# Kernel tuning notes

Measured on AMD Instinct MI355X. Metric: run time of the kernel, lower is better.

## Reference

```python
import jax, jax.numpy as jnp
import numpy as np

DIM = 1280
HEADS = 8
DH = DIM // HEADS  # 160
CROSS = 768
FRAMES = 16
B = 2
TOK = 256        # spatial tokens per frame
ESEQ = 77
INNER = 4 * DIM  # 5120, geglu inner


def _ln(x, w, b):
    m = x.mean(-1, keepdims=True)
    v = x.var(-1, keepdims=True)
    return (x - m) / jnp.sqrt(v + 1e-5) * w + b


def _split_heads(x):
    Bt, S, C = x.shape
    return x.reshape(Bt, S, HEADS, C // HEADS).transpose(0, 2, 1, 3)


def _attn_core(q, k, v):
    # q,k,v: [B, S, C] -> multi-head attention -> [B, Sq, C]
    qh, kh, vh = _split_heads(q), _split_heads(k), _split_heads(v)
    scores = jnp.einsum('bhqd,bhkd->bhqk', qh, kh) * (DH ** -0.5)
    attn = jax.nn.softmax(scores, axis=-1)
    o = jnp.einsum('bhqk,bhkd->bhqd', attn, vh)
    Bt, H, S, Dh = o.shape
    return o.transpose(0, 2, 1, 3).reshape(Bt, S, H * Dh)


def setup_inputs() -> dict:
    key = jax.random.key(0)
    ks = jax.random.split(key, 32)
    s = 0.02

    def w(i, shape):
        return jax.random.normal(ks[i], shape, dtype=jnp.float32) * s

    inp = {
        'hidden_states': jax.random.normal(ks[0], (B * FRAMES, TOK, DIM), dtype=jnp.float32),
        'encoder_hidden_states': jax.random.normal(ks[1], (B * FRAMES, ESEQ, CROSS), dtype=jnp.float32),
        # norm1 / attn1 (sparse causal self-attn)
        'n1w': jnp.ones((DIM,), jnp.float32), 'n1b': jnp.zeros((DIM,), jnp.float32),
        'a1wq': w(2, (DIM, DIM)), 'a1wk': w(3, (DIM, DIM)), 'a1wv': w(4, (DIM, DIM)),
        'a1wo': w(5, (DIM, DIM)), 'a1bo': jnp.zeros((DIM,), jnp.float32),
        # norm2 / attn2 (cross)
        'n2w': jnp.ones((DIM,), jnp.float32), 'n2b': jnp.zeros((DIM,), jnp.float32),
        'a2wq': w(6, (DIM, DIM)), 'a2wk': w(7, (CROSS, DIM)), 'a2wv': w(8, (CROSS, DIM)),
        'a2wo': w(9, (DIM, DIM)), 'a2bo': jnp.zeros((DIM,), jnp.float32),
        # norm3 / geglu FFN
        'n3w': jnp.ones((DIM,), jnp.float32), 'n3b': jnp.zeros((DIM,), jnp.float32),
        'ffw1': w(10, (DIM, 2 * INNER)), 'ffb1': jnp.zeros((2 * INNER,), jnp.float32),
        'ffw2': w(11, (INNER, DIM)), 'ffb2': jnp.zeros((DIM,), jnp.float32),
        # norm_temp / attn_temp (temporal self-attn)
        'ntw': jnp.ones((DIM,), jnp.float32), 'ntb': jnp.zeros((DIM,), jnp.float32),
        'atwq': w(12, (DIM, DIM)), 'atwk': w(13, (DIM, DIM)), 'atwv': w(14, (DIM, DIM)),
        'atwo': w(15, (DIM, DIM)), 'atbo': jnp.zeros((DIM,), jnp.float32),
        'video_length': FRAMES,
    }
    return inp


def reference(hidden_states, encoder_hidden_states,
              n1w, n1b, a1wq, a1wk, a1wv, a1wo, a1bo,
              n2w, n2b, a2wq, a2wk, a2wv, a2wo, a2bo,
              n3w, n3b, ffw1, ffb1, ffw2, ffb2,
              ntw, ntb, atwq, atwk, atwv, atwo, atbo,
              video_length):
    f = video_length
    bf, d, c = hidden_states.shape
    b = bf // f
    h = hidden_states

    # ---- attn1: sparse causal self-attention ----
    nh = _ln(h, n1w, n1b)
    q = nh @ a1wq                                   # [bf, d, c]
    k = (nh @ a1wk).reshape(b, f, d, c)
    v = (nh @ a1wv).reshape(b, f, d, c)
    former = jnp.maximum(jnp.arange(f) - 1, 0)      # clamp(arange-1, min=0)
    k_sel = jnp.concatenate([jnp.broadcast_to(k[:, :1], (b, f, d, c)), k[:, former]], axis=2)
    v_sel = jnp.concatenate([jnp.broadcast_to(v[:, :1], (b, f, d, c)), v[:, former]], axis=2)
    k_sel = k_sel.reshape(bf, 2 * d, c)
    v_sel = v_sel.reshape(bf, 2 * d, c)
    h = _attn_core(q, k_sel, v_sel) @ a1wo + a1bo + h

    # ---- attn2: cross-attention to text ----
    nh = _ln(h, n2w, n2b)
    h = _attn_core(nh @ a2wq, encoder_hidden_states @ a2wk, encoder_hidden_states @ a2wv) @ a2wo + a2bo + h

    # ---- geglu FFN ----
    nh = _ln(h, n3w, n3b)
    pg = nh @ ffw1 + ffb1
    p, g = jnp.split(pg, 2, axis=-1)
    h = (p * jax.nn.gelu(g, approximate=False)) @ ffw2 + ffb2 + h

    # ---- temporal self-attention over frames ----
    ht = h.reshape(b, f, d, c).transpose(0, 2, 1, 3).reshape(b * d, f, c)
    nh = _ln(ht, ntw, ntb)
    ht = _attn_core(nh @ atwq, nh @ atwk, nh @ atwv) @ atwo + atbo + ht
    h = ht.reshape(b, d, f, c).transpose(0, 2, 1, 3).reshape(bf, d, c)
    return h
```

## Files before the change

kernel.cpp:

```cpp
#include <hip/hip_runtime.h>
#include <hip/hip_bf16.h>
#include <math.h>

#define DIM    1280
#define HEADS  8
#define DH     160
#define FRAMES 16
#define BATCH  2
#define TOK    256
#define ESEQ   77
#define INNER  5120
#define CROSS  768
#define BF     (BATCH*FRAMES)
#define ROWS   (BF*TOK)
#define EROWS  (BF*ESEQ)
#define EPAD   2560

typedef __hip_bfloat16 bf16;
typedef __attribute__((ext_vector_type(8))) short s8v;
typedef __attribute__((ext_vector_type(4))) short s4v;
typedef __attribute__((ext_vector_type(4))) float f4v;

__device__ __forceinline__ float us2f(unsigned short u) {
    union { float f; unsigned int i; } c; c.i = ((unsigned int)u) << 16; return c.f;
}
__device__ __forceinline__ float b2f(bf16 x) { return __bfloat162float(x); }
__device__ __forceinline__ bf16  f2b(float x) { return __float2bfloat16(x); }
__device__ __forceinline__ short f2s(float x) {
    union { float f; unsigned int u; } c; c.f = x;
    unsigned int r = c.u + 0x7FFF + ((c.u >> 16) & 1);
    return (short)(r >> 16);
}
__device__ __forceinline__ void load4(const float* p, float* d) {
    float4 v = *(const float4*)p; d[0] = v.x; d[1] = v.y; d[2] = v.z; d[3] = v.w;
}
__device__ __forceinline__ void gl_lds16(const bf16* g, short* l) {
    __builtin_amdgcn_global_load_lds(
        (const __attribute__((address_space(1))) void*)g,
        (__attribute__((address_space(3))) void*)l, 16, 0, 0);
}

__global__ __launch_bounds__(256) void ln_kernel(const float* __restrict__ x,
                                                 const float* __restrict__ w,
                                                 const float* __restrict__ b,
                                                 bf16* __restrict__ out) {
    __shared__ float r1[256], r2[256];
    int row = blockIdx.x, t = threadIdx.x;
    const float* xp = x + (size_t)row * DIM;
    float v[5], s = 0.f, s2 = 0.f;
#pragma unroll
    for (int i = 0; i < 5; i++) {
        float xv = xp[t + 256 * i];
        v[i] = xv; s += xv; s2 += xv * xv;
    }
    r1[t] = s; r2[t] = s2; __syncthreads();
    for (int st = 128; st > 0; st >>= 1) {
        if (t < st) { r1[t] += r1[t + st]; r2[t] += r2[t + st]; }
        __syncthreads();
    }
    float mean = r1[0] * (1.f / DIM);
    float var  = r2[0] * (1.f / DIM) - mean * mean;
    float rstd = rsqrtf(var + 1e-5f);
    bf16* op = out + (size_t)row * DIM;
#pragma unroll
    for (int i = 0; i < 5; i++) {
        int c = t + 256 * i;
        op[c] = f2b((v[i] - mean) * rstd * w[c] + b[c]);
    }
}

__global__ __launch_bounds__(256) void wconv_t(const float* __restrict__ w,
                                               bf16* __restrict__ wt,
                                               int N, int K) {
    __shared__ float tile[64][65];
    const int n0 = blockIdx.x * 64, k0 = blockIdx.y * 64;
    const int t = threadIdx.x;
    const int tr = t >> 4;
    const int tc = (t & 15) * 4;
#pragma unroll
    for (int i = 0; i < 4; i++) {
        int kk = tr + i * 16;
        float4 vv = *(const float4*)(w + (size_t)(k0 + kk) * N + n0 + tc);
        tile[kk][tc + 0] = vv.x; tile[kk][tc + 1] = vv.y;
        tile[kk][tc + 2] = vv.z; tile[kk][tc + 3] = vv.w;
    }
    __syncthreads();
#pragma unroll
    for (int i = 0; i < 4; i++) {
        int nn = tr + i * 16;
        s4v o4 = (s4v){ f2s(tile[tc + 0][nn]), f2s(tile[tc + 1][nn]),
                        f2s(tile[tc + 2][nn]), f2s(tile[tc + 3][nn]) };
        *(s4v*)(wt + (size_t)(n0 + nn) * K + k0 + tc) = o4;
    }
}

__global__ __launch_bounds__(256) void wconv_t4(const float* __restrict__ w0,
                                                const float* __restrict__ w1,
                                                const float* __restrict__ w2,
                                                const float* __restrict__ w3,
                                                bf16* __restrict__ wt, size_t dstride,
                                                int N, int K) {
    const float* w = blockIdx.z == 0 ? w0 : blockIdx.z == 1 ? w1
                   : blockIdx.z == 2 ? w2 : w3;
    bf16* dst = wt + (size_t)blockIdx.z * dstride;
    __shared__ float tile[64][65];
    const int n0 = blockIdx.x * 64, k0 = blockIdx.y * 64;
    const int t = threadIdx.x;
    const int tr = t >> 4;
    const int tc = (t & 15) * 4;
#pragma unroll
    for (int i = 0; i < 4; i++) {
        int kk = tr + i * 16;
        float4 vv = *(const float4*)(w + (size_t)(k0 + kk) * N + n0 + tc);
        tile[kk][tc + 0] = vv.x; tile[kk][tc + 1] = vv.y;
        tile[kk][tc + 2] = vv.z; tile[kk][tc + 3] = vv.w;
    }
    __syncthreads();
#pragma unroll
    for (int i = 0; i < 4; i++) {
        int nn = tr + i * 16;
        s4v o4 = (s4v){ f2s(tile[tc + 0][nn]), f2s(tile[tc + 1][nn]),
                        f2s(tile[tc + 2][nn]), f2s(tile[tc + 3][nn]) };
        *(s4v*)(dst + (size_t)(n0 + nn) * K + k0 + tc) = o4;
    }
}

__global__ __launch_bounds__(256) void encconv(const float* __restrict__ e,
                                               bf16* __restrict__ eb) {
    int idx = blockIdx.x * 256 + threadIdx.x;
    int base = idx * 4;
    int row = base / CROSS;
    s4v o4;
    if (row < EROWS) {
        float4 vv = *(const float4*)(e + (size_t)base);
        o4 = (s4v){ f2s(vv.x), f2s(vv.y), f2s(vv.z), f2s(vv.w) };
    } else {
        o4 = (s4v){ 0, 0, 0, 0 };
    }
    *(s4v*)(eb + base) = o4;
}

template <int EPI>
__global__ __launch_bounds__(256) void gemm_bt(
    const bf16* __restrict__ A, int lda,
    const bf16* __restrict__ Bt, int ldb,
    void* __restrict__ C, int ldc,
    const float* __restrict__ bias,
    const float* __restrict__ res, int ldres,
    int M, int N, int K) {
    constexpr int BN = (EPI == 2) ? 64 : 128;
    constexpr int MI = (EPI == 2) ? 2 : 4;
    __shared__ short A_lds[2][128 * 32];
    __shared__ short B_lds[2][BN * 32];
    __shared__ short G_lds[EPI == 2 ? 2 * 64 * 32 : 8];

    const int t = threadIdx.x;
    const int wid = t >> 6, lane = t & 63;
    const int lrow = lane & 15, lgrp = lane >> 4;
    const int m0 = blockIdx.y * 128, n0 = blockIdx.x * BN;
    const int wm = (EPI == 2) ? wid * 32 : (wid & 1) * 64;
    const int wn = (EPI == 2) ? 0 : (wid >> 1) * 64;

    f4v acc[MI][4];
    f4v accg[EPI == 2 ? MI : 1][4];
#pragma unroll
    for (int i = 0; i < MI; i++)
#pragma unroll
        for (int j = 0; j < 4; j++) {
            acc[i][j] = (f4v){0.f, 0.f, 0.f, 0.f};
            if (EPI == 2) accg[i][j] = (f4v){0.f, 0.f, 0.f, 0.f};
        }

    const int scol = (lane & 3) * 8;
    const int arow = wid * 32 + (lane >> 2);
    const int brow = (EPI == 2) ? (wid * 16 + (lane >> 2)) : arow;
    const bf16* Ag0 = A + (size_t)(m0 + arow) * lda + scol;
    const bf16* Bg0 = Bt + (size_t)(n0 + brow) * ldb + scol;
    const bf16* Gg0 = (EPI == 2) ? (Bt + (size_t)(INNER + n0 + brow) * ldb + scol) : Bg0;

    auto stage = [&](int buf, int kk) {
        gl_lds16(Ag0 + kk, &A_lds[buf][wid * 1024]);
        gl_lds16(Ag0 + kk + (size_t)16 * lda, &A_lds[buf][wid * 1024 + 512]);
        if constexpr (EPI == 2) {
            gl_lds16(Bg0 + kk, &B_lds[buf][wid * 512]);
            gl_lds16(Gg0 + kk, &G_lds[buf * 2048 + wid * 512]);
        } else {
            gl_lds16(Bg0 + kk, &B_lds[buf][wid * 1024]);
            gl_lds16(Bg0 + kk + (size_t)16 * ldb, &B_lds[buf][wid * 1024 + 512]);
        }
    };

    stage(0, 0);
    __syncthreads();
    int buf = 0;
    for (int k0 = 0; k0 < K; k0 += 32, buf ^= 1) {
        if (k0 + 32 < K) stage(buf ^ 1, k0 + 32);

        s8v af[MI], bfr[4];
#pragma unroll
        for (int i = 0; i < MI; i++)
            af[i] = *(const s8v*)&A_lds[buf][(wm + i * 16 + lrow) * 32 + lgrp * 8];
#pragma unroll
        for (int j = 0; j < 4; j++)
            bfr[j] = *(const s8v*)&B_lds[buf][(wn + j * 16 + lrow) * 32 + lgrp * 8];
#pragma unroll
        for (int i = 0; i < MI; i++)
#pragma unroll
            for (int j = 0; j < 4; j++)
                acc[i][j] = __builtin_amdgcn_mfma_f32_16x16x32_bf16(af[i], bfr[j], acc[i][j], 0, 0, 0);
        if constexpr (EPI == 2) {
            s8v gfr[4];
#pragma unroll
            for (int j = 0; j < 4; j++)
                gfr[j] = *(const s8v*)&G_lds[buf * 2048 + (j * 16 + lrow) * 32 + lgrp * 8];
#pragma unroll
            for (int i = 0; i < MI; i++)
#pragma unroll
                for (int j = 0; j < 4; j++)
                    accg[i][j] = __builtin_amdgcn_mfma_f32_16x16x32_bf16(af[i], gfr[j], accg[i][j], 0, 0, 0);
        }
        __syncthreads();
    }

#pragma unroll
    for (int i = 0; i < MI; i++) {
#pragma unroll
        for (int r = 0; r < 4; r++) {
            int m = m0 + wm + i * 16 + lgrp * 4 + r;
#pragma unroll
            for (int j = 0; j < 4; j++) {
                int n = n0 + wn + j * 16 + lrow;
                float v = acc[i][j][r];
                if (EPI == 0) {
                    ((bf16*)C)[(size_t)m * ldc + n] = f2b(v);
                } else if (EPI == 1) {
                    v += bias[n] + res[(size_t)m * ldres + n];
                    ((float*)C)[(size_t)m * ldc + n] = v;
                } else {
                    float p = v + bias[n];
                    float g = accg[i][j][r] + bias[INNER + n];
                    float gl = 0.5f * g * (1.f + erff(g * 0.70710678118654752f));
                    ((bf16*)C)[(size_t)m * ldc + n] = f2b(p * gl);
                }
            }
        }
    }
}

template <int EPI>
__global__ __launch_bounds__(256) void gemm_mfma(
    const bf16* __restrict__ A, int lda,
    const float* __restrict__ B, int ldb,
    void* __restrict__ C, int ldc,
    const float* __restrict__ bias,
    const float* __restrict__ res, int ldres,
    int M, int N, int K) {
    constexpr int LR = 40;
    __shared__ short A_lds[128 * LR];
    __shared__ short B_lds[128 * LR];
    __shared__ short G_lds[EPI == 2 ? 128 * LR : 4];

    const int t    = threadIdx.x;
    const int wid  = t >> 6, lane = t & 63;
    const int lrow = lane & 15, lgrp = lane >> 4;
    const int m0   = blockIdx.y * 128, n0 = blockIdx.x * 128;
    const int wm   = (wid & 1) * 64, wn = (wid >> 1) * 64;

    f4v acc[4][4];
    f4v accg[4][4];
#pragma unroll
    for (int i = 0; i < 4; i++)
#pragma unroll
        for (int j = 0; j < 4; j++) {
            acc[i][j] = (f4v){0.f, 0.f, 0.f, 0.f};
            if (EPI == 2) accg[i][j] = (f4v){0.f, 0.f, 0.f, 0.f};
        }

    const int b_np = (t & 31) * 4;
    const int b_kp = (t >> 5) * 4;

    for (int k0 = 0; k0 < K; k0 += 32) {
#pragma unroll
        for (int c = 0; c < 2; c++) {
            int idx = t + c * 256;
            int row = idx >> 2, g = (idx & 3) * 8;
            uint4 v = *(const uint4*)(A + (size_t)(m0 + row) * lda + k0 + g);
            *(uint4*)&A_lds[row * LR + g] = v;
        }
        {
            const float* bp = B + (size_t)(k0 + b_kp) * ldb + n0 + b_np;
            float4 r0 = *(const float4*)(bp);
            float4 r1 = *(const float4*)(bp + ldb);
            float4 r2 = *(const float4*)(bp + 2 * ldb);
            float4 r3 = *(const float4*)(bp + 3 * ldb);
            *(s4v*)&B_lds[(b_np + 0) * LR + b_kp] = (s4v){f2s(r0.x), f2s(r1.x), f2s(r2.x), f2s(r3.x)};
            *(s4v*)&B_lds[(b_np + 1) * LR + b_kp] = (s4v){f2s(r0.y), f2s(r1.y), f2s(r2.y), f2s(r3.y)};
            *(s4v*)&B_lds[(b_np + 2) * LR + b_kp] = (s4v){f2s(r0.z), f2s(r1.z), f2s(r2.z), f2s(r3.z)};
            *(s4v*)&B_lds[(b_np + 3) * LR + b_kp] = (s4v){f2s(r0.w), f2s(r1.w), f2s(r2.w), f2s(r3.w)};
        }
        if (EPI == 2) {
            const float* gp = B + (size_t)(k0 + b_kp) * ldb + INNER + n0 + b_np;
            float4 r0 = *(const float4*)(gp);
            float4 r1 = *(const float4*)(gp + ldb);
            float4 r2 = *(const float4*)(gp + 2 * ldb);
            float4 r3 = *(const float4*)(gp + 3 * ldb);
            *(s4v*)&G_lds[(b_np + 0) * LR + b_kp] = (s4v){f2s(r0.x), f2s(r1.x), f2s(r2.x), f2s(r3.x)};
            *(s4v*)&G_lds[(b_np + 1) * LR + b_kp] = (s4v){f2s(r0.y), f2s(r1.y), f2s(r2.y), f2s(r3.y)};
            *(s4v*)&G_lds[(b_np + 2) * LR + b_kp] = (s4v){f2s(r0.z), f2s(r1.z), f2s(r2.z), f2s(r3.z)};
            *(s4v*)&G_lds[(b_np + 3) * LR + b_kp] = (s4v){f2s(r0.w), f2s(r1.w), f2s(r2.w), f2s(r3.w)};
        }
        __syncthreads();
        s8v af[4], bfr[4];
#pragma unroll
        for (int i = 0; i < 4; i++)
            af[i] = *(const s8v*)&A_lds[(wm + i * 16 + lrow) * LR + lgrp * 8];
#pragma unroll
        for (int j = 0; j < 4; j++)
            bfr[j] = *(const s8v*)&B_lds[(wn + j * 16 + lrow) * LR + lgrp * 8];
#pragma unroll
        for (int i = 0; i < 4; i++)
#pragma unroll
            for (int j = 0; j < 4; j++)
                acc[i][j] = __builtin_amdgcn_mfma_f32_16x16x32_bf16(af[i], bfr[j], acc[i][j], 0, 0, 0);
        if (EPI == 2) {
            s8v gfr[4];
#pragma unroll
            for (int j = 0; j < 4; j++)
                gfr[j] = *(const s8v*)&G_lds[(wn + j * 16 + lrow) * LR + lgrp * 8];
#pragma unroll
            for (int i = 0; i < 4; i++)
#pragma unroll
                for (int j = 0; j < 4; j++)
                    accg[i][j] = __builtin_amdgcn_mfma_f32_16x16x32_bf16(af[i], gfr[j], accg[i][j], 0, 0, 0);
        }
        __syncthreads();
    }
#pragma unroll
    for (int i = 0; i < 4; i++) {
#pragma unroll
        for (int r = 0; r < 4; r++) {
            int m = m0 + wm + i * 16 + lgrp * 4 + r;
#pragma unroll
            for (int j = 0; j < 4; j++) {
                int n = n0 + wn + j * 16 + lrow;
                float v = acc[i][j][r];
                if (EPI == 0) {
                    ((bf16*)C)[(size_t)m * ldc + n] = f2b(v);
                } else if (EPI == 1) {
                    v += bias[n] + res[(size_t)m * ldres + n];
                    ((float*)C)[(size_t)m * ldc + n] = v;
                } else {
                    float p = v + bias[n];
                    float g = accg[i][j][r] + bias[INNER + n];
                    float gl = 0.5f * g * (1.f + erff(g * 0.70710678118654752f));
                    ((bf16*)C)[(size_t)m * ldc + n] = f2b(p * gl);
                }
            }
        }
    }
}

__global__ __launch_bounds__(256) void gemm_valu(
    const float* __restrict__ A, int lda,
    const float* __restrict__ B, int ldb,
    bf16* __restrict__ C, int ldc,
    int M, int N, int K) {
    __shared__ float As[16][65];
    __shared__ float Bs[16][65];
    const int t  = threadIdx.x;
    const int m0 = blockIdx.y * 64, n0 = blockIdx.x * 64;
    const int ar = t >> 2, ak = (t & 3) * 4;
    const int bk = t >> 4, bn = (t & 15) * 4;
    const int ty = t >> 4, tx = t & 15;
    float acc[4][4];
#pragma unroll
    for (int i = 0; i < 4; i++)
#pragma unroll
        for (int j = 0; j < 4; j++) acc[i][j] = 0.f;

    for (int k0 = 0; k0 < K; k0 += 16) {
        {
            int m = m0 + ar;
            float tmp[4];
            if (m < M) load4(A + (size_t)m * lda + k0 + ak, tmp);
            else { tmp[0] = tmp[1] = tmp[2] = tmp[3] = 0.f; }
            As[ak + 0][ar] = tmp[0]; As[ak + 1][ar] = tmp[1];
            As[ak + 2][ar] = tmp[2]; As[ak + 3][ar] = tmp[3];
        }
        {
            float tmp[4];
            load4(B + (size_t)(k0 + bk) * ldb + n0 + bn, tmp);
            Bs[bk][bn + 0] = tmp[0]; Bs[bk][bn + 1] = tmp[1];
            Bs[bk][bn + 2] = tmp[2]; Bs[bk][bn + 3] = tmp[3];
        }
        __syncthreads();
#pragma unroll
        for (int k = 0; k < 16; k++) {
            float a[4], b[4];
#pragma unroll
            for (int i = 0; i < 4; i++) a[i] = As[k][ty * 4 + i];
#pragma unroll
            for (int j = 0; j < 4; j++) b[j] = Bs[k][tx * 4 + j];
#pragma unroll
            for (int i = 0; i < 4; i++)
#pragma unroll
                for (int j = 0; j < 4; j++) acc[i][j] += a[i] * b[j];
        }
        __syncthreads();
    }
#pragma unroll
    for (int i = 0; i < 4; i++) {
        int m = m0 + ty * 4 + i;
        if (m >= M) continue;
#pragma unroll
        for (int j = 0; j < 4; j++) {
            int n = n0 + tx * 4 + j;
            C[(size_t)m * ldc + n] = f2b(acc[i][j]);
        }
    }
}

#define SOFTMAX_SCALE 0.07905694150420949f

#define A1_KP 168
#define A1_VP 72
#define A1_PP 72

__global__ __launch_bounds__(256) void attn1_mfma(const bf16* __restrict__ q,
                                                  const bf16* __restrict__ k,
                                                  const bf16* __restrict__ v,
                                                  int ldq,
                                                  bf16* __restrict__ o) {
    __shared__ short K_lds[64 * A1_KP];
    __shared__ short Vt_lds[160 * A1_VP];
    __shared__ short P_lds[4 * 16 * A1_PP];

    const int t = threadIdx.x;
    const int wid = t >> 6, lane = t & 63;
    const int lrow = lane & 15, lgrp = lane >> 4;
    const int bx = blockIdx.x, hd = blockIdx.y, bfi = blockIdx.z;
    const int bi = bfi >> 4, fi = bfi & 15;
    const int former = fi > 0 ? fi - 1 : 0;
    const int qrow0 = bfi * TOK + bx * 64 + wid * 16;

    s8v qf[5];
    {
        const bf16* qp = q + (size_t)(qrow0 + lrow) * ldq + hd * DH + lgrp * 8;
#pragma unroll
        for (int ks = 0; ks < 5; ks++)
            qf[ks] = *(const s8v*)(qp + ks * 32);
    }

    f4v oacc[10];
#pragma unroll
    for (int dg = 0; dg < 10; dg++) oacc[dg] = (f4v){0.f, 0.f, 0.f, 0.f};
    float m_run[4], l_run[4];
#pragma unroll
    for (int r = 0; r < 4; r++) { m_run[r] = -1e30f; l_run[r] = 0.f; }

    short* P_w = P_lds + wid * 16 * A1_PP;

    for (int c = 0; c < 8; c++) {
        const int kf = (c < 4) ? 0 : former;
        const size_t krow0 = (size_t)(bi * FRAMES + kf) * TOK + (c & 3) * 64;

        __syncthreads();
#pragma unroll
        for (int it = 0; it < 5; it++) {
            int idx = t + it * 256;
            int jr = idx / 20, g = idx % 20;
            const bf16* kp = k + (krow0 + jr) * ldq + hd * DH + g * 8;
            *(uint4*)&K_lds[jr * A1_KP + g * 8] = *(const uint4*)kp;
            s8v vv = *(const s8v*)(v + (krow0 + jr) * ldq + hd * DH + g * 8);
#pragma unroll
            for (int i = 0; i < 8; i++) {
                int d = g * 8 + i;
                Vt_lds[d * A1_VP + (jr ^ (d & 56))] = vv[i];
            }
        }
        __syncthreads();

        f4v sacc[4];
#pragma unroll
        for (int kg = 0; kg < 4; kg++) {
            sacc[kg] = (f4v){0.f, 0.f, 0.f, 0.f};
#pragma unroll
            for (int ks = 0; ks < 5; ks++) {
                s8v kfr = *(const s8v*)&K_lds[(kg * 16 + lrow) * A1_KP + ks * 32 + lgrp * 8];
                sacc[kg] = __builtin_amdgcn_mfma_f32_16x16x32_bf16(qf[ks], kfr, sacc[kg], 0, 0, 0);
            }
        }

        float mc[4];
#pragma unroll
        for (int r = 0; r < 4; r++) {
            float mm = fmaxf(fmaxf(sacc[0][r], sacc[1][r]), fmaxf(sacc[2][r], sacc[3][r]));
            mc[r] = mm * SOFTMAX_SCALE;
        }
#pragma unroll
        for (int x = 1; x < 16; x <<= 1)
#pragma unroll
            for (int r = 0; r < 4; r++)
                mc[r] = fmaxf(mc[r], __shfl_xor(mc[r], x));

        float p[4][4], rs[4];
#pragma unroll
        for (int r = 0; r < 4; r++) {
            float mn = fmaxf(m_run[r], mc[r]);
            float sc = __expf(m_run[r] - mn);
            m_run[r] = mn;
            l_run[r] *= sc;
#pragma unroll
            for (int dg = 0; dg < 10; dg++) oacc[dg][r] *= sc;
            float acc = 0.f;
#pragma unroll
            for (int kg = 0; kg < 4; kg++) {
                float e = __expf(sacc[kg][r] * SOFTMAX_SCALE - mn);
                p[kg][r] = e; acc += e;
            }
            rs[r] = acc;
        }
#pragma unroll
        for (int x = 1; x < 16; x <<= 1)
#pragma unroll
            for (int r = 0; r < 4; r++)
                rs[r] += __shfl_xor(rs[r], x);
#pragma unroll
        for (int r = 0; r < 4; r++) l_run[r] += rs[r];

#pragma unroll
        for (int kg = 0; kg < 4; kg++)
#pragma unroll
            for (int r = 0; r < 4; r++)
                P_w[(lgrp * 4 + r) * A1_PP + kg * 16 + lrow] = f2s(p[kg][r]);
        __syncthreads();

        s8v pa[2];
#pragma unroll
        for (int ks2 = 0; ks2 < 2; ks2++)
            pa[ks2] = *(const s8v*)&P_w[lrow * A1_PP + ks2 * 32 + lgrp * 8];
#pragma unroll
        for (int dg = 0; dg < 10; dg++) {
            int dd = dg * 16 + lrow;
#pragma unroll
            for (int ks2 = 0; ks2 < 2; ks2++) {
                s8v vfr = *(const s8v*)&Vt_lds[dd * A1_VP + ((ks2 * 32 + lgrp * 8) ^ (dd & 56))];
                oacc[dg] = __builtin_amdgcn_mfma_f32_16x16x32_bf16(pa[ks2], vfr, oacc[dg], 0, 0, 0);
            }
        }
    }

    float invl[4];
#pragma unroll
    for (int r = 0; r < 4; r++) invl[r] = 1.f / l_run[r];
#pragma unroll
    for (int dg = 0; dg < 10; dg++) {
#pragma unroll
        for (int r = 0; r < 4; r++) {
            int qq = qrow0 + lgrp * 4 + r;
            o[(size_t)qq * DIM + hd * DH + dg * 16 + lrow] = f2b(oacc[dg][r] * invl[r]);
        }
    }
}

__global__ __launch_bounds__(256) void attn2_mfma(const bf16* __restrict__ q,
                                                  const bf16* __restrict__ k,
                                                  const bf16* __restrict__ v,
                                                  int ldk,
                                                  bf16* __restrict__ o) {
    __shared__ short K_lds[64 * A1_KP];
    __shared__ short Vt_lds[160 * A1_VP];
    __shared__ short P_lds[4 * 16 * A1_PP];

    const int t = threadIdx.x;
    const int wid = t >> 6, lane = t & 63;
    const int lrow = lane & 15, lgrp = lane >> 4;
    const int bx = blockIdx.x, hd = blockIdx.y, bfi = blockIdx.z;
    const int qrow0 = bfi * TOK + bx * 64 + wid * 16;

    s8v qf[5];
    {
        const bf16* qp = q + (size_t)(qrow0 + lrow) * DIM + hd * DH + lgrp * 8;
#pragma unroll
        for (int ks = 0; ks < 5; ks++)
            qf[ks] = *(const s8v*)(qp + ks * 32);
    }

    f4v oacc[10];
#pragma unroll
    for (int dg = 0; dg < 10; dg++) oacc[dg] = (f4v){0.f, 0.f, 0.f, 0.f};
    float m_run[4], l_run[4];
#pragma unroll
    for (int r = 0; r < 4; r++) { m_run[r] = -1e30f; l_run[r] = 0.f; }

    short* P_w = P_lds + wid * 16 * A1_PP;

    for (int c = 0; c < 2; c++) {
        const size_t krow0 = (size_t)bfi * ESEQ + c * 64;

        __syncthreads();
#pragma unroll
        for (int it = 0; it < 5; it++) {
            int idx = t + it * 256;
            int jr = idx / 20, g = idx % 20;
            const bf16* kp = k + (krow0 + jr) * ldk + hd * DH + g * 8;
            *(uint4*)&K_lds[jr * A1_KP + g * 8] = *(const uint4*)kp;
            s8v vv = *(const s8v*)(v + (krow0 + jr) * ldk + hd * DH + g * 8);
#pragma unroll
            for (int i = 0; i < 8; i++) {
                int d = g * 8 + i;
                Vt_lds[d * A1_VP + (jr ^ (d & 56))] = vv[i];
            }
        }
        __syncthreads();

        f4v sacc[4];
#pragma unroll
        for (int kg = 0; kg < 4; kg++) {
            sacc[kg] = (f4v){0.f, 0.f, 0.f, 0.f};
#pragma unroll
            for (int ks = 0; ks < 5; ks++) {
                s8v kfr = *(const s8v*)&K_lds[(kg * 16 + lrow) * A1_KP + ks * 32 + lgrp * 8];
                sacc[kg] = __builtin_amdgcn_mfma_f32_16x16x32_bf16(qf[ks], kfr, sacc[kg], 0, 0, 0);
            }
            if (c == 1 && (kg > 0 || lrow >= 13))
                sacc[kg] = (f4v){-1e30f, -1e30f, -1e30f, -1e30f};
        }

        float mc[4];
#pragma unroll
        for (int r = 0; r < 4; r++) {
            float mm = fmaxf(fmaxf(sacc[0][r], sacc[1][r]), fmaxf(sacc[2][r], sacc[3][r]));
            mc[r] = mm * SOFTMAX_SCALE;
        }
#pragma unroll
        for (int x = 1; x < 16; x <<= 1)
#pragma unroll
            for (int r = 0; r < 4; r++)
                mc[r] = fmaxf(mc[r], __shfl_xor(mc[r], x));

        float p[4][4], rs[4];
#pragma unroll
        for (int r = 0; r < 4; r++) {
            float mn = fmaxf(m_run[r], mc[r]);
            float sc = __expf(m_run[r] - mn);
            m_run[r] = mn;
            l_run[r] *= sc;
#pragma unroll
            for (int dg = 0; dg < 10; dg++) oacc[dg][r] *= sc;
            float acc = 0.f;
#pragma unroll
            for (int kg = 0; kg < 4; kg++) {
                float e = __expf(sacc[kg][r] * SOFTMAX_SCALE - mn);
                p[kg][r] = e; acc += e;
            }
            rs[r] = acc;
        }
#pragma unroll
        for (int x = 1; x < 16; x <<= 1)
#pragma unroll
            for (int r = 0; r < 4; r++)
                rs[r] += __shfl_xor(rs[r], x);
#pragma unroll
        for (int r = 0; r < 4; r++) l_run[r] += rs[r];

#pragma unroll
        for (int kg = 0; kg < 4; kg++)
#pragma unroll
            for (int r = 0; r < 4; r++)
                P_w[(lgrp * 4 + r) * A1_PP + kg * 16 + lrow] = f2s(p[kg][r]);
        __syncthreads();

        s8v pa[2];
#pragma unroll
        for (int ks2 = 0; ks2 < 2; ks2++)
            pa[ks2] = *(const s8v*)&P_w[lrow * A1_PP + ks2 * 32 + lgrp * 8];
#pragma unroll
        for (int dg = 0; dg < 10; dg++) {
            int dd = dg * 16 + lrow;
#pragma unroll
            for (int ks2 = 0; ks2 < 2; ks2++) {
                s8v vfr = *(const s8v*)&Vt_lds[dd * A1_VP + ((ks2 * 32 + lgrp * 8) ^ (dd & 56))];
                oacc[dg] = __builtin_amdgcn_mfma_f32_16x16x32_bf16(pa[ks2], vfr, oacc[dg], 0, 0, 0);
            }
        }
    }

    float invl[4];
#pragma unroll
    for (int r = 0; r < 4; r++) invl[r] = 1.f / l_run[r];
#pragma unroll
    for (int dg = 0; dg < 10; dg++) {
#pragma unroll
        for (int r = 0; r < 4; r++) {
            int qq = qrow0 + lgrp * 4 + r;
            o[(size_t)qq * DIM + hd * DH + dg * 16 + lrow] = f2b(oacc[dg][r] * invl[r]);
        }
    }
}

__global__ __launch_bounds__(256) void attn2_kernel(const bf16* __restrict__ q,
                                                    const bf16* __restrict__ k,
                                                    const bf16* __restrict__ v,
                                                    bf16* __restrict__ o) {
    __shared__ float sQ[DH];
    __shared__ float sS[128];
    __shared__ float red[256];
    int t = threadIdx.x;
    int qi = blockIdx.x, hd = blockIdx.y, bfi = blockIdx.z;
    size_t qbase = ((size_t)(bfi * TOK + qi)) * DIM + hd * DH;
    if (t < DH) sQ[t] = b2f(q[qbase + t]);
    __syncthreads();
    if (t < ESEQ) {
        size_t kbase = ((size_t)(bfi * ESEQ + t)) * DIM + hd * DH;
        float acc = 0.f;
        for (int d = 0; d < DH; d++) acc += sQ[d] * b2f(k[kbase + d]);
        sS[t] = acc * SOFTMAX_SCALE;
    }
    __syncthreads();
    float lm = (t < ESEQ) ? sS[t] : -1e30f;
    red[t] = lm; __syncthreads();
    for (int s = 128; s > 0; s >>= 1) { if (t < s) red[t] = fmaxf(red[t], red[t + s]); __syncthreads(); }
    float mx = red[0]; __syncthreads();
    float ls = 0.f;
    if (t < ESEQ) { float e = __expf(sS[t] - mx); sS[t] = e; ls = e; }
    red[t] = ls; __syncthreads();
    for (int s = 128; s > 0; s >>= 1) { if (t < s) red[t] += red[t + s]; __syncthreads(); }
    float inv = 1.f / red[0];
    __syncthreads();
    if (t < DH) {
        float acc = 0.f;
        for (int j = 0; j < ESEQ; j++) {
            size_t vbase = ((size_t)(bfi * ESEQ + j)) * DIM + hd * DH;
            acc += sS[j] * b2f(v[vbase + t]);
        }
        o[qbase + t] = f2b(acc * inv);
    }
}

#define AT_P 168
__global__ __launch_bounds__(256) void attnt_vec(const bf16* __restrict__ q,
                                                 const bf16* __restrict__ k,
                                                 const bf16* __restrict__ v,
                                                 int ldq,
                                                 bf16* __restrict__ o) {
    __shared__ short Q_l[16 * AT_P], K_l[16 * AT_P], V_l[16 * AT_P];
    __shared__ float P_l[16][17];
    const int t = threadIdx.x;
    const int hd = blockIdx.y;
    const int z = blockIdx.x;
    const int bi = z >> 8, ti = z & 255;

#pragma unroll
    for (int it = 0; it < 2; it++) {
        int c = t + it * 256;
        if (c < 320) {
            int f = c / 20, g = c % 20;
            size_t row = (size_t)(bi * FRAMES + f) * TOK + ti;
            const bf16* qp = q + row * ldq + hd * DH + g * 8;
            const bf16* kp = k + row * ldq + hd * DH + g * 8;
            const bf16* vp = v + row * ldq + hd * DH + g * 8;
            *(uint4*)&Q_l[f * AT_P + g * 8] = *(const uint4*)qp;
            *(uint4*)&K_l[f * AT_P + g * 8] = *(const uint4*)kp;
            *(uint4*)&V_l[f * AT_P + g * 8] = *(const uint4*)vp;
        }
    }
    __syncthreads();

    const int fq = t >> 4, fk = t & 15;
    float acc = 0.f;
#pragma unroll
    for (int dg = 0; dg < 20; dg++) {
        s8v qv = *(const s8v*)&Q_l[fq * AT_P + dg * 8];
        s8v kv = *(const s8v*)&K_l[fk * AT_P + dg * 8];
#pragma unroll
        for (int e = 0; e < 8; e++)
            acc += us2f((unsigned short)qv[e]) * us2f((unsigned short)kv[e]);
    }
    acc *= SOFTMAX_SCALE;
    float mx = acc;
#pragma unroll
    for (int x = 1; x < 16; x <<= 1) mx = fmaxf(mx, __shfl_xor(mx, x));
    float ex = __expf(acc - mx);
    float sm = ex;
#pragma unroll
    for (int x = 1; x < 16; x <<= 1) sm += __shfl_xor(sm, x);
    P_l[fq][fk] = ex / sm;
    __syncthreads();

#pragma unroll
    for (int it = 0; it < 2; it++) {
        int a = t + it * 256;
        if (a < 320) {
            int pq = a & 15, dg = a >> 4;
            float pr[16];
#pragma unroll
            for (int j = 0; j < 16; j++) pr[j] = P_l[pq][j];
            float ov[8] = {0.f, 0.f, 0.f, 0.f, 0.f, 0.f, 0.f, 0.f};
#pragma unroll
            for (int j = 0; j < 16; j++) {
                s8v vv = *(const s8v*)&V_l[j * AT_P + dg * 8];
#pragma unroll
                for (int i = 0; i < 8; i++)
                    ov[i] += pr[j] * us2f((unsigned short)vv[i]);
            }
            s8v o8;
#pragma unroll
            for (int i = 0; i < 8; i++) o8[i] = f2s(ov[i]);
            size_t orow = (size_t)(bi * FRAMES + pq) * TOK + ti;
            *(s8v*)(o + orow * DIM + hd * DH + dg * 8) = o8;
        }
    }
}

__global__ __launch_bounds__(256) void attnt_kernel(const bf16* __restrict__ q,
                                                    const bf16* __restrict__ k,
                                                    const bf16* __restrict__ v,
                                                    int ldq,
                                                    bf16* __restrict__ o) {
    __shared__ float sQ[DH];
    __shared__ float sS[16];
    __shared__ float red[256];
    int t = threadIdx.x;
    int qfi = blockIdx.x, hd = blockIdx.y, z = blockIdx.z;
    int bi = z >> 8, ti = z & 255;
    size_t qrow = (size_t)(bi * FRAMES + qfi) * TOK + ti;
    if (t < DH) sQ[t] = b2f(q[qrow * ldq + hd * DH + t]);
    __syncthreads();
    if (t < FRAMES) {
        size_t krow = (size_t)(bi * FRAMES + t) * TOK + ti;
        float acc = 0.f;
        for (int d = 0; d < DH; d++) acc += sQ[d] * b2f(k[krow * ldq + hd * DH + d]);
        sS[t] = acc * SOFTMAX_SCALE;
    }
    __syncthreads();
    float lm = (t < FRAMES) ? sS[t] : -1e30f;
    red[t] = lm; __syncthreads();
    for (int s = 128; s > 0; s >>= 1) { if (t < s) red[t] = fmaxf(red[t], red[t + s]); __syncthreads(); }
    float mx = red[0]; __syncthreads();
    float ls = 0.f;
    if (t < FRAMES) { float e = __expf(sS[t] - mx); sS[t] = e; ls = e; }
    red[t] = ls; __syncthreads();
    for (int s = 128; s > 0; s >>= 1) { if (t < s) red[t] += red[t + s]; __syncthreads(); }
    float inv = 1.f / red[0];
    __syncthreads();
    if (t < DH) {
        float acc = 0.f;
        for (int j = 0; j < FRAMES; j++) {
            size_t vrow = (size_t)(bi * FRAMES + j) * TOK + ti;
            acc += sS[j] * b2f(v[vrow * ldq + hd * DH + t]);
        }
        o[qrow * DIM + hd * DH + t] = f2b(acc * inv);
    }
}

extern "C" void kernel_launch(void* const* d_in, const int* in_sizes, int n_in,
                              void* d_out, int out_size, void* d_ws, size_t ws_size,
                              hipStream_t stream) {
    (void)in_sizes; (void)n_in; (void)out_size;
    const float* hs   = (const float*)d_in[0];
    const float* enc  = (const float*)d_in[1];
    const float* n1w  = (const float*)d_in[2];
    const float* n1b  = (const float*)d_in[3];
    const float* a1wq = (const float*)d_in[4];
    const float* a1wk = (const float*)d_in[5];
    const float* a1wv = (const float*)d_in[6];
    const float* a1wo = (const float*)d_in[7];
    const float* a1bo = (const float*)d_in[8];
    const float* n2w  = (const float*)d_in[9];
    const float* n2b  = (const float*)d_in[10];
    const float* a2wq = (const float*)d_in[11];
    const float* a2wk = (const float*)d_in[12];
    const float* a2wv = (const float*)d_in[13];
    const float* a2wo = (const float*)d_in[14];
    const float* a2bo = (const float*)d_in[15];
    const float* n3w  = (const float*)d_in[16];
    const float* n3b  = (const float*)d_in[17];
    const float* ffw1 = (const float*)d_in[18];
    const float* ffb1 = (const float*)d_in[19];
    const float* ffw2 = (const float*)d_in[20];
    const float* ffb2 = (const float*)d_in[21];
    const float* ntw  = (const float*)d_in[22];
    const float* ntb  = (const float*)d_in[23];
    const float* atwq = (const float*)d_in[24];
    const float* atwk = (const float*)d_in[25];
    const float* atwv = (const float*)d_in[26];
    const float* atwo = (const float*)d_in[27];
    const float* atbo = (const float*)d_in[28];

    char* wp = (char*)d_ws;
    auto carve = [&](size_t bytes) -> char* {
        char* p = wp; wp += (bytes + 255) & ~((size_t)255); return p;
    };
    const size_t BUF = (size_t)ROWS * DIM * 2;
    const size_t W_FULL = 26214400;
    float* out = (float*)d_out;
    dim3 blk(256);

    bf16* nh = (bf16*)carve(BUF);

    bool full = (ws_size >= 5 * BUF + W_FULL + 4096);
    if (!full) {
        bf16* qb = (bf16*)carve(BUF);
        bf16* kb = (bf16*)carve(BUF);
        bf16* vb = (bf16*)carve(BUF);
        bf16* ob = (bf16*)carve(BUF);
        bf16* Pb = qb;
        auto proj = [&](const bf16* A, int lda, const float* B, int ldb,
                        bf16* C, int ldc, int M, int N, int K) {
            gemm_mfma<0><<<dim3(N / 128, M / 128), blk, 0, stream>>>(
                A, lda, B, ldb, C, ldc, nullptr, nullptr, 0, M, N, K);
        };
        auto outproj = [&](const bf16* A, int lda, const float* B,
                           const float* bias, const float* res, int K) {
            gemm_mfma<1><<<dim3(DIM / 128, ROWS / 128), blk, 0, stream>>>(
                A, lda, B, DIM, out, DIM, bias, res, DIM, ROWS, DIM, K);
        };
        ln_kernel<<<dim3(ROWS), blk, 0, stream>>>(hs, n1w, n1b, nh);
        proj(nh, DIM, a1wq, DIM, qb, DIM, ROWS, DIM, DIM);
        proj(nh, DIM, a1wk, DIM, kb, DIM, ROWS, DIM, DIM);
        proj(nh, DIM, a1wv, DIM, vb, DIM, ROWS, DIM, DIM);
        attn1_mfma<<<dim3(TOK / 64, HEADS, BF), blk, 0, stream>>>(qb, kb, vb, DIM, ob);
        outproj(ob, DIM, a1wo, a1bo, hs, DIM);

        ln_kernel<<<dim3(ROWS), blk, 0, stream>>>(out, n2w, n2b, nh);
        proj(nh, DIM, a2wq, DIM, qb, DIM, ROWS, DIM, DIM);
        gemm_valu<<<dim3(DIM / 64, (EROWS + 63) / 64), blk, 0, stream>>>(enc, CROSS, a2wk, DIM, kb, DIM, EROWS, DIM, CROSS);
        gemm_valu<<<dim3(DIM / 64, (EROWS + 63) / 64), blk, 0, stream>>>(enc, CROSS, a2wv, DIM, vb, DIM, EROWS, DIM, CROSS);
        attn2_kernel<<<dim3(TOK, HEADS, BF), blk, 0, stream>>>(qb, kb, vb, ob);
        outproj(ob, DIM, a2wo, a2bo, out, DIM);

        ln_kernel<<<dim3(ROWS), blk, 0, stream>>>(out, n3w, n3b, nh);
        gemm_mfma<2><<<dim3(INNER / 128, ROWS / 128), blk, 0, stream>>>(
            nh, DIM, ffw1, 2 * INNER, Pb, INNER, ffb1, nullptr, 0, ROWS, INNER, DIM);
        outproj(Pb, INNER, ffw2, ffb2, out, INNER);

        ln_kernel<<<dim3(ROWS), blk, 0, stream>>>(out, ntw, ntb, nh);
        proj(nh, DIM, atwq, DIM, qb, DIM, ROWS, DIM, DIM);
        proj(nh, DIM, atwk, DIM, kb, DIM, ROWS, DIM, DIM);
        proj(nh, DIM, atwv, DIM, vb, DIM, ROWS, DIM, DIM);
        attnt_kernel<<<dim3(FRAMES, HEADS, BATCH * TOK), blk, 0, stream>>>(qb, kb, vb, DIM, ob);
        outproj(ob, DIM, atwo, atbo, out, DIM);
        return;
    }

    bf16* C3 = (bf16*)carve(3 * BUF);
    bf16* ob = (bf16*)carve(BUF);
    bf16* Ws = (bf16*)carve(W_FULL);
    bf16* Pb = C3;
    const size_t WQ = (size_t)DIM * DIM;
    const size_t WC = (size_t)DIM * CROSS;
    const int LDQ3 = 3 * DIM;

    auto projN = [&](const bf16* A, int lda, const bf16* Bt, int ldb,
                     bf16* C, int ldc, int M, int N, int K) {
        gemm_bt<0><<<dim3(N / 128, M / 128), blk, 0, stream>>>(
            A, lda, Bt, ldb, C, ldc, nullptr, nullptr, 0, M, N, K);
    };
    auto outprojN = [&](const bf16* A, int lda, const bf16* Bt, int ldb,
                        const float* bias, const float* res, int K) {
        gemm_bt<1><<<dim3(DIM / 128, ROWS / 128), blk, 0, stream>>>(
            A, lda, Bt, ldb, out, DIM, bias, res, DIM, ROWS, DIM, K);
    };

    wconv_t4<<<dim3(DIM / 64, DIM / 64, 4), blk, 0, stream>>>(
        a1wq, a1wk, a1wv, a1wo, Ws, WQ, DIM, DIM);
    ln_kernel<<<dim3(ROWS), blk, 0, stream>>>(hs, n1w, n1b, nh);
    projN(nh, DIM, Ws, DIM, C3, LDQ3, ROWS, 3 * DIM, DIM);
    attn1_mfma<<<dim3(TOK / 64, HEADS, BF), blk, 0, stream>>>(
        C3, C3 + DIM, C3 + 2 * DIM, LDQ3, ob);
    outprojN(ob, DIM, Ws + 3 * WQ, DIM, a1bo, hs, DIM);

    {
        bf16* w2q  = Ws;
        bf16* w2o  = Ws + WQ;
        bf16* w2k  = Ws + 2 * WQ;
        bf16* w2v  = w2k + WC;
        bf16* encb = w2v + WC;
        bf16* qb2  = C3;
        bf16* kv2  = C3 + (size_t)ROWS * DIM;
        wconv_t4<<<dim3(DIM / 64, DIM / 64, 2), blk, 0, stream>>>(
            a2wq, a2wo, nullptr, nullptr, w2q, WQ, DIM, DIM);
        wconv_t4<<<dim3(DIM / 64, CROSS / 64, 2), blk, 0, stream>>>(
            a2wk, a2wv, nullptr, nullptr, w2k, WC, DIM, CROSS);
        encconv<<<dim3(EPAD * CROSS / 1024), blk, 0, stream>>>(enc, encb);
        ln_kernel<<<dim3(ROWS), blk, 0, stream>>>(out, n2w, n2b, nh);
        projN(nh, DIM, w2q, DIM, qb2, DIM, ROWS, DIM, DIM);
        projN(encb, CROSS, w2k, CROSS, kv2, 2 * DIM, EPAD, 2 * DIM, CROSS);
        attn2_mfma<<<dim3(TOK / 64, HEADS, BF), blk, 0, stream>>>(
            qb2, kv2, kv2 + DIM, 2 * DIM, ob);
        outprojN(ob, DIM, w2o, DIM, a2bo, out, DIM);
    }

    wconv_t<<<dim3(2 * INNER / 64, DIM / 64), blk, 0, stream>>>(ffw1, Ws, 2 * INNER, DIM);
    ln_kernel<<<dim3(ROWS), blk, 0, stream>>>(out, n3w, n3b, nh);
    gemm_bt<2><<<dim3(INNER / 64, ROWS / 128), blk, 0, stream>>>(
        nh, DIM, Ws, DIM, Pb, INNER, ffb1, nullptr, 0, ROWS, INNER, DIM);
    wconv_t<<<dim3(DIM / 64, INNER / 64), blk, 0, stream>>>(ffw2, Ws, DIM, INNER);
    gemm_bt<1><<<dim3(DIM / 128, ROWS / 128), blk, 0, stream>>>(
        Pb, INNER, Ws, INNER, out, DIM, ffb2, out, DIM, ROWS, DIM, INNER);

    wconv_t4<<<dim3(DIM / 64, DIM / 64, 4), blk, 0, stream>>>(
        atwq, atwk, atwv, atwo, Ws, WQ, DIM, DIM);
    ln_kernel<<<dim3(ROWS), blk, 0, stream>>>(out, ntw, ntb, nh);
    projN(nh, DIM, Ws, DIM, C3, LDQ3, ROWS, 3 * DIM, DIM);
    attnt_vec<<<dim3(BATCH * TOK, HEADS), blk, 0, stream>>>(
        C3, C3 + DIM, C3 + 2 * DIM, LDQ3, ob);
    outprojN(ob, DIM, Ws + 3 * WQ, DIM, atbo, out, DIM);
}
```

Measured before the change: 1.391 ms.

## Add 256x256-tile 512-thread bf16 MFMA GEMM for projections and FFN down-proj

Introduces gemm_bt8, a GEMM with 256x256 output tiles, 8 waves and a K-step of 64. It uses double-buffered global-to-LDS loads with an XOR-style column swizzle. The kernel replaces the 128x128 gemm_bt for the QKV, cross-attention and output projections and for the FFN second GEMM. The goal is more operand reuse per LDS byte and fewer global loads per FLOP. The trade-off is 128KB of LDS per block and fewer blocks: 160 for N=1280, which is below the CU count and may leave the device underfilled.

```diff
diff --git a/kernel.cpp b/kernel.cpp
--- a/kernel.cpp
+++ b/kernel.cpp
@@ -138,6 +138,91 @@
         o4 = (s4v){ 0, 0, 0, 0 };
     }
     *(s4v*)(eb + base) = o4;
+}
+
+template <int EPI>
+__global__ __launch_bounds__(512, 2) void gemm_bt8(
+    const bf16* __restrict__ A, int lda,
+    const bf16* __restrict__ Bt, int ldb,
+    void* __restrict__ C, int ldc,
+    const float* __restrict__ bias,
+    const float* __restrict__ res, int ldres,
+    int M, int N, int K) {
+    __shared__ short lds[2][2][256 * 64];
+
+    const int t = threadIdx.x;
+    const int wid = t >> 6, lane = t & 63;
+    const int lrow = lane & 15, lgrp = lane >> 4;
+    const int wr = wid >> 2, wc = wid & 3;
+    const int m0 = blockIdx.y * 256, n0 = blockIdx.x * 256;
+
+    f4v acc[8][4];
+#pragma unroll
+    for (int i = 0; i < 8; i++)
+#pragma unroll
+        for (int j = 0; j < 4; j++) acc[i][j] = (f4v){0.f, 0.f, 0.f, 0.f};
+
+    const int srow = wid * 32 + (lane >> 3);
+    const int scol = (((lane & 7) - (lane >> 3)) & 7) * 8;
+    const bf16* Ag = A + (size_t)(m0 + srow) * lda + scol;
+    const bf16* Bg = Bt + (size_t)(n0 + srow) * ldb + scol;
+
+    auto stage = [&](int b, int kt) {
+#pragma unroll
+        for (int s = 0; s < 4; s++) {
+            gl_lds16(Ag + (size_t)kt * 64 + (size_t)(s * 8) * lda,
+                     &lds[b][0][wid * 2048 + s * 512]);
+            gl_lds16(Bg + (size_t)kt * 64 + (size_t)(s * 8) * ldb,
+                     &lds[b][1][wid * 2048 + s * 512]);
+        }
+    };
+
+    const int KT = K >> 6;
+    stage(0, 0);
+    __syncthreads();
+    int buf = 0;
+    for (int kt = 0; kt < KT; kt++, buf ^= 1) {
+        if (kt + 1 < KT) stage(buf ^ 1, kt + 1);
+#pragma unroll
+        for (int ks = 0; ks < 2; ks++) {
+            const int cc = ((ks * 4 + lgrp + lrow) & 7) * 8;
+            s8v bfr[4];
+#pragma unroll
+            for (int j = 0; j < 4; j++)
+                bfr[j] = *(const s8v*)&lds[buf][1][(wc * 64 + j * 16 + lrow) * 64 + cc];
+#pragma unroll
+            for (int i = 0; i < 8; i++) {
+                s8v af = *(const s8v*)&lds[buf][0][(wr * 128 + i * 16 + lrow) * 64 + cc];
+#pragma unroll
+                for (int j = 0; j < 4; j++)
+                    acc[i][j] = __builtin_amdgcn_mfma_f32_16x16x32_bf16(af, bfr[j], acc[i][j], 0, 0, 0);
+            }
+        }
+        __syncthreads();
+    }
+
+    float bs[4];
+    if (EPI == 1) {
+#pragma unroll
+        for (int j = 0; j < 4; j++) bs[j] = bias[n0 + wc * 64 + j * 16 + lrow];
+    }
+#pragma unroll
+    for (int i = 0; i < 8; i++) {
+#pragma unroll
+        for (int r = 0; r < 4; r++) {
+            int m = m0 + wr * 128 + i * 16 + lgrp * 4 + r;
+#pragma unroll
+            for (int j = 0; j < 4; j++) {
+                int n = n0 + wc * 64 + j * 16 + lrow;
+                float v = acc[i][j][r];
+                if (EPI == 0) {
+                    ((bf16*)C)[(size_t)m * ldc + n] = f2b(v);
+                } else {
+                    ((float*)C)[(size_t)m * ldc + n] = v + bs[j] + res[(size_t)m * ldres + n];
+                }
+            }
+        }
+    }
 }
 
 template <int EPI>
@@ -896,6 +981,7 @@
     const size_t W_FULL = 26214400;
     float* out = (float*)d_out;
     dim3 blk(256);
+    dim3 blk8(512);
 
     bf16* nh = (bf16*)carve(BUF);
 
@@ -954,12 +1040,12 @@
 
     auto projN = [&](const bf16* A, int lda, const bf16* Bt, int ldb,
                      bf16* C, int ldc, int M, int N, int K) {
-        gemm_bt<0><<<dim3(N / 128, M / 128), blk, 0, stream>>>(
+        gemm_bt8<0><<<dim3(N / 256, M / 256), blk8, 0, stream>>>(
             A, lda, Bt, ldb, C, ldc, nullptr, nullptr, 0, M, N, K);
     };
     auto outprojN = [&](const bf16* A, int lda, const bf16* Bt, int ldb,
                         const float* bias, const float* res, int K) {
-        gemm_bt<1><<<dim3(DIM / 128, ROWS / 128), blk, 0, stream>>>(
+        gemm_bt8<1><<<dim3(DIM / 256, ROWS / 256), blk8, 0, stream>>>(
             A, lda, Bt, ldb, out, DIM, bias, res, DIM, ROWS, DIM, K);
     };
 
@@ -997,7 +1083,7 @@
     gemm_bt<2><<<dim3(INNER / 64, ROWS / 128), blk, 0, stream>>>(
         nh, DIM, Ws, DIM, Pb, INNER, ffb1, nullptr, 0, ROWS, INNER, DIM);
     wconv_t<<<dim3(DIM / 64, INNER / 64), blk, 0, stream>>>(ffw2, Ws, DIM, INNER);
-    gemm_bt<1><<<dim3(DIM / 128, ROWS / 128), blk, 0, stream>>>(
+    gemm_bt8<1><<<dim3(DIM / 256, ROWS / 256), blk8, 0, stream>>>(
         Pb, INNER, Ws, INNER, out, DIM, ffb2, out, DIM, ROWS, DIM, INNER);
 
     wconv_t4<<<dim3(DIM / 64, DIM / 64, 4), blk, 0, stream>>>(
```

New measurement: 1.191 ms. 14.4% less time.
